# Optimization experiments

Measured on AMD Instinct MI355X. Metric: run time of the kernel, lower is better.

The kernel has to match this reference:

```python
import jax, jax.numpy as jnp
from jax import lax
import numpy as np

BETA = 0.5
ITERATION = 50
K = 1
EPS = 1e-5  # F.normalize eps


def cost_matrix_cosine(x, y):
    # x: [b,m,d], y: [b,n,d] -> cosine distance [b,m,n]
    xn = x / jnp.maximum(jnp.linalg.norm(x, axis=-1, keepdims=True), EPS)
    yn = y / jnp.maximum(jnp.linalg.norm(y, axis=-1, keepdims=True), EPS)
    return 1.0 - jnp.einsum('bmd,bnd->bmn', xn, yn)


def ipot(C, x_len, x_pad, y_len, y_pad, joint_pad, beta, iteration, k):
    # C: [b,m,n]; x_*: txt (m); y_*: img (n). Returns transport plan [b,m,n].
    b, m, n = C.shape
    jp_t = jnp.transpose(joint_pad, (0, 2, 1))                      # [b,n,m]
    A = jnp.where(jp_t, 0.0, jnp.exp(-jnp.transpose(C, (0, 2, 1)) / beta))
    T0 = jnp.where(jp_t, 0.0, 1.0)                                  # [b,n,m]
    sigma0 = jnp.where(x_pad, 0.0, 1.0 / x_len[:, None])[:, :, None]  # [b,m,1]
    x_mask = (x_pad.astype(C.dtype) * 1e4)[:, None, :]              # [b,1,m]
    y_mask = (y_pad.astype(C.dtype) * 1e4)[:, None, :]              # [b,1,n]
    xl = x_len[:, None, None]
    yl = y_len[:, None, None]

    def outer(carry, _):
        T, sigma = carry
        Q = A * T                                                   # [b,n,m]
        def inner(sig, _):
            # sig: [b,m,1]
            delta = 1.0 / (yl * jnp.transpose(jnp.matmul(Q, sig), (0, 2, 1)) + y_mask)  # [b,1,n]
            sig = jnp.transpose(1.0 / (xl * jnp.matmul(delta, Q) + x_mask), (0, 2, 1))  # [b,m,1]
            return sig, delta
        sigma, deltas = lax.scan(inner, sigma, None, length=k)
        delta = deltas[-1]                                          # [b,1,n]
        T = jnp.transpose(delta, (0, 2, 1)) * Q * jnp.transpose(sigma, (0, 2, 1))  # [b,n,m]
        return (T, sigma), None

    (T, _), _ = lax.scan(outer, (T0, sigma0), None, length=iteration)
    return jnp.transpose(T, (0, 2, 1))                              # [b,m,n]


def optimal_transport_dist(txt_emb, img_emb, txt_pad, img_pad):
    cost = cost_matrix_cosine(txt_emb, img_emb)                     # [b,m,n]
    joint_pad = txt_pad[:, :, None] | img_pad[:, None, :]           # [b,m,n]
    cost = jnp.where(joint_pad, 0.0, cost)
    txt_len = (txt_pad.shape[1] - jnp.sum(txt_pad, axis=1)).astype(cost.dtype)
    img_len = (img_pad.shape[1] - jnp.sum(img_pad, axis=1)).astype(cost.dtype)
    T = ipot(lax.stop_gradient(cost), txt_len, txt_pad, img_len, img_pad,
             joint_pad, BETA, ITERATION, K)
    # trace(cost @ T^T) == sum_ij cost_ij * plan_ij, per sample
    return jnp.sum(cost * lax.stop_gradient(T), axis=(1, 2))        # [b]


def reference(entitytxt_vec, object_vec, entitytxt_num, object_num):
    txt_nodes_emb = entitytxt_vec.astype(jnp.float32)               # [b,tl,d]
    img_nodes_emb = object_vec[:, 1:].astype(jnp.float32)           # [b,il,d]
    txt_pad = entitytxt_num == 0                                    # [b,tl] bool
    img_pad = object_num[:, 1:] == 0                                # [b,il] bool
    ot_dist = optimal_transport_dist(txt_nodes_emb, img_nodes_emb, txt_pad, img_pad)
    ot_loss = jnp.sum(ot_dist) * 0.01
    return ot_loss


def setup_inputs():
    key = jax.random.key(0)
    k1, k2, k3, k4 = jax.random.split(key, 4)
    b, tl, il1, d = 256, 128, 128, 1024
    entitytxt_vec = jax.random.normal(k1, (b, tl, d), dtype=jnp.float32)
    object_vec = jax.random.normal(k2, (b, il1, d), dtype=jnp.float32)
    entitytxt_num = jax.random.randint(k3, (b, tl), 0, 2, dtype=jnp.int32)
    object_num = jax.random.randint(k4, (b, il1), 0, 2, dtype=jnp.int32)
    # guarantee at least one valid node per sample (avoid 1/0 lengths)
    entitytxt_num = entitytxt_num.at[:, 0].set(1)
    object_num = object_num.at[:, 1].set(1)
    return {"entitytxt_vec": entitytxt_vec, "object_vec": object_vec,
            "entitytxt_num": entitytxt_num, "object_num": object_num}
```

## Files before the change

### kernel.cpp

```cpp
#include <hip/hip_runtime.h>
#include <math.h>

#define BATCH 256
#define M 128
#define NIMG 127
#define NP 128
#define D 1024
#define BK 64
#define NT (D / BK)
#define ITERS 50
#define LROW 72

typedef __attribute__((ext_vector_type(8))) short bf16x8;
typedef __attribute__((ext_vector_type(4))) float floatx4;

static __device__ __forceinline__ unsigned pack_bf16x2(float a, float b) {
    unsigned ua = __builtin_bit_cast(unsigned, a);
    unsigned ub = __builtin_bit_cast(unsigned, b);
    ua += 0x7fffu + ((ua >> 16) & 1u);
    ub += 0x7fffu + ((ub >> 16) & 1u);
    return (ua >> 16) | (ub & 0xffff0000u);
}

template<int CTRL>
static __device__ __forceinline__ float dpp_add(float v) {
    int s = __builtin_amdgcn_update_dpp(0, __builtin_bit_cast(int, v), CTRL, 0xf, 0xf, true);
    return v + __builtin_bit_cast(float, s);
}
static __device__ __forceinline__ float red16(float v) {
    v = dpp_add<0x121>(v);
    v = dpp_add<0x122>(v);
    v = dpp_add<0x124>(v);
    v = dpp_add<0x128>(v);
    return v;
}

static __device__ __forceinline__ void load_tile(const float* __restrict__ xb,
                                                 const float* __restrict__ yb,
                                                 int kk, int r0, int c16,
                                                 float4 (&vx)[4], float4 (&vy)[4]) {
#pragma unroll
    for (int it = 0; it < 4; ++it) {
        const int r = r0 + it * 32;
        vx[it] = *(const float4*)(xb + (size_t)r * D + kk + c16 * 4);
        float4 z = make_float4(0.f, 0.f, 0.f, 0.f);
        if (r < NIMG) z = *(const float4*)(yb + (size_t)r * D + kk + c16 * 4);
        vy[it] = z;
    }
}

static __device__ __forceinline__ void stage_tile(short* __restrict__ Xs, short* __restrict__ Ys,
                                                  int r0, int c16,
                                                  const float4 (&vx)[4], const float4 (&vy)[4],
                                                  float (&ssx)[4], float (&ssy)[4]) {
#pragma unroll
    for (int it = 0; it < 4; ++it) {
        const int r = r0 + it * 32;
        float4 v = vx[it];
        ssx[it] = fmaf(v.x, v.x, fmaf(v.y, v.y, fmaf(v.z, v.z, fmaf(v.w, v.w, ssx[it]))));
        uint2 p;
        p.x = pack_bf16x2(v.x, v.y);
        p.y = pack_bf16x2(v.z, v.w);
        *(uint2*)(&Xs[r * LROW + c16 * 4]) = p;
        v = vy[it];
        ssy[it] = fmaf(v.x, v.x, fmaf(v.y, v.y, fmaf(v.z, v.z, fmaf(v.w, v.w, ssy[it]))));
        p.x = pack_bf16x2(v.x, v.y);
        p.y = pack_bf16x2(v.z, v.w);
        *(uint2*)(&Ys[r * LROW + c16 * 4]) = p;
    }
}

static __device__ __forceinline__ void mfma_tile(const short* __restrict__ Xs,
                                                 const short* __restrict__ Ys,
                                                 int mbase, int nbase, int col, int quad,
                                                 floatx4 (&acc)[2][4]) {
#pragma unroll
    for (int ks = 0; ks < 2; ++ks) {
        const int koff = ks * 32 + quad * 8;
        bf16x8 af[2], bfr[4];
#pragma unroll
        for (int tr = 0; tr < 2; ++tr)
            af[tr] = *(const bf16x8*)(&Xs[(mbase + tr * 16 + col) * LROW + koff]);
#pragma unroll
        for (int tc = 0; tc < 4; ++tc)
            bfr[tc] = *(const bf16x8*)(&Ys[(nbase + tc * 16 + col) * LROW + koff]);
#pragma unroll
        for (int tr = 0; tr < 2; ++tr)
#pragma unroll
            for (int tc = 0; tc < 4; ++tc)
                acc[tr][tc] = __builtin_amdgcn_mfma_f32_16x16x32_bf16(
                    af[tr], bfr[tc], acc[tr][tc], 0, 0, 0);
    }
}

__launch_bounds__(512, 1)
__global__ void gemm_a_kernel(const float* __restrict__ xg,
                              const float* __restrict__ yg,
                              const int* __restrict__ xnum,
                              const int* __restrict__ ynum,
                              float* __restrict__ Aout)
{
    __shared__ __align__(16) short Xs[M * LROW];
    __shared__ __align__(16) short Ys[M * LROW];
    __shared__ __align__(16) float sinvx[M];
    __shared__ __align__(16) float sinvy[NP];
    __shared__ __align__(16) float sxmask[M];
    __shared__ __align__(16) float symask[NP];

    const int b    = blockIdx.x;
    const int t    = threadIdx.x;
    const int lane = t & 63;
    const int w    = t >> 6;

    const float* xb = xg + (size_t)b * M * D;
    const float* yb = yg + ((size_t)b * 128 + 1) * D;

    if (t < M)  sxmask[t] = (xnum[b * M + t] == 0) ? 1.0f : 0.0f;
    if (t < NP) symask[t] = (t < NIMG && ynum[b * 128 + t + 1] != 0) ? 0.0f : 1.0f;

    const int r0  = t >> 4;
    const int c16 = t & 15;

    floatx4 acc[2][4];
#pragma unroll
    for (int a = 0; a < 2; ++a)
#pragma unroll
        for (int c = 0; c < 4; ++c) acc[a][c] = (floatx4)0.0f;

    float ssx[4] = {0.f, 0.f, 0.f, 0.f};
    float ssy[4] = {0.f, 0.f, 0.f, 0.f};

    const int mbase = (w & 3) * 32;
    const int nbase = (w >> 2) * 64;
    const int col   = lane & 15;
    const int quad  = lane >> 4;

    float4 vxa[4], vya[4], vxb[4], vyb[4];
    load_tile(xb, yb, 0, r0, c16, vxa, vya);

#pragma unroll 1
    for (int ii = 0; ii < NT; ii += 2) {
        stage_tile(Xs, Ys, r0, c16, vxa, vya, ssx, ssy);
        load_tile(xb, yb, (ii + 1) * BK, r0, c16, vxb, vyb);
        __syncthreads();
        mfma_tile(Xs, Ys, mbase, nbase, col, quad, acc);
        __syncthreads();
        stage_tile(Xs, Ys, r0, c16, vxb, vyb, ssx, ssy);
        if (ii + 2 < NT) load_tile(xb, yb, (ii + 2) * BK, r0, c16, vxa, vya);
        __syncthreads();
        mfma_tile(Xs, Ys, mbase, nbase, col, quad, acc);
        __syncthreads();
    }

#pragma unroll
    for (int it = 0; it < 4; ++it) {
        ssx[it] = red16(ssx[it]);
        ssy[it] = red16(ssy[it]);
    }
    if (c16 == 0) {
#pragma unroll
        for (int it = 0; it < 4; ++it) {
            const int r = r0 + it * 32;
            sinvx[r] = 1.0f / fmaxf(sqrtf(ssx[it]), 1e-5f);
            sinvy[r] = 1.0f / fmaxf(sqrtf(ssy[it]), 1e-5f);
        }
    }
    __syncthreads();

    float* Ab = Aout + (size_t)b * M * NP;
#pragma unroll
    for (int tr = 0; tr < 2; ++tr)
#pragma unroll
        for (int tc = 0; tc < 4; ++tc) {
            const int n = nbase + tc * 16 + col;
            const float ivy_n = sinvy[n];
            const float ymf   = symask[n];
#pragma unroll
            for (int reg = 0; reg < 4; ++reg) {
                const int m = mbase + tr * 16 + quad * 4 + reg;
                const float p = acc[tr][tc][reg] * sinvx[m] * ivy_n;
                const float a = (sxmask[m] + ymf > 0.0f) ? 0.0f : expf(2.0f * p - 2.0f);
                Ab[m * NP + n] = a;
            }
        }
}

__launch_bounds__(512, 1)
__global__ void ipot_kernel(const float* __restrict__ Ain,
                            const int* __restrict__ xnum,
                            const int* __restrict__ ynum,
                            float* __restrict__ out)
{
    __shared__ __align__(16) float partCS[8 * 128];
    __shared__ __align__(16) float sdelta[NP];
    __shared__ __align__(16) float ssigma[M];
    __shared__ __align__(16) float sxmask[M];
    __shared__ __align__(16) float symask[NP];
    __shared__ float sxl_s, syl_s;
    __shared__ unsigned scnt[16];
    __shared__ float swsum[8];

    const int b    = blockIdx.x;
    const int t    = threadIdx.x;
    const int lane = t & 63;
    const int w    = t >> 6;
    const int tj   = t & 15;
    const int i0   = (t >> 4) * 4;
    const int j0   = tj * 8;

    bool tpad = true, ipad = true;
    if (t < M)  { tpad = (xnum[b * M + t] == 0); sxmask[t] = tpad ? 1e4f : 0.0f; }
    if (t < NP) { ipad = !(t < NIMG && ynum[b * 128 + t + 1] != 0); symask[t] = ipad ? 1e4f : 0.0f; }
    unsigned long long bx = __ballot(t < M  && !tpad);
    unsigned long long by = __ballot(t < NP && !ipad);
    if (lane == 0) { scnt[w] = (unsigned)__popcll(bx); scnt[8 + w] = (unsigned)__popcll(by); }
    __syncthreads();
    if (t == 0) {
        float xl = 0.f, yl = 0.f;
        for (int k = 0; k < 8; ++k) { xl += scnt[k]; yl += scnt[8 + k]; }
        sxl_s = xl; syl_s = yl;
    }
    __syncthreads();
    const float xl = sxl_s, yl = syl_s;
    if (t < M) ssigma[t] = tpad ? 0.0f : __builtin_amdgcn_rcpf(xl);

    const float* Ab = Ain + (size_t)b * M * NP;
    float Af[4][8], Q[4][8];
#pragma unroll
    for (int r = 0; r < 4; ++r) {
        float4 a0 = *(const float4*)(Ab + (size_t)(i0 + r) * NP + j0);
        float4 a1 = *(const float4*)(Ab + (size_t)(i0 + r) * NP + j0 + 4);
        Af[r][0] = a0.x; Af[r][1] = a0.y; Af[r][2] = a0.z; Af[r][3] = a0.w;
        Af[r][4] = a1.x; Af[r][5] = a1.y; Af[r][6] = a1.z; Af[r][7] = a1.w;
#pragma unroll
        for (int j = 0; j < 8; ++j) Q[r][j] = Af[r][j];
    }
    __syncthreads();

    float lp = 0.0f;
    for (int itn = 0; itn < ITERS; ++itn) {
        float sg[4];
        *(float4*)sg = *(const float4*)(&ssigma[i0]);
        float cp[8] = {0.f,0.f,0.f,0.f,0.f,0.f,0.f,0.f};
#pragma unroll
        for (int r = 0; r < 4; ++r)
#pragma unroll
            for (int j = 0; j < 8; ++j)
                cp[j] = fmaf(sg[r], Q[r][j], cp[j]);
#pragma unroll
        for (int j = 0; j < 8; ++j) {
            cp[j] += __shfl_xor(cp[j], 16);
            cp[j] += __shfl_xor(cp[j], 32);
        }
        if (lane < 16) {
            float4 c0 = make_float4(cp[0], cp[1], cp[2], cp[3]);
            float4 c1 = make_float4(cp[4], cp[5], cp[6], cp[7]);
            *(float4*)(&partCS[w * 128 + tj * 8])     = c0;
            *(float4*)(&partCS[w * 128 + tj * 8 + 4]) = c1;
        }
        __syncthreads();
        if (t < NP) {
            float s = 0.f;
#pragma unroll
            for (int w8 = 0; w8 < 8; ++w8) s += partCS[w8 * 128 + t];
            sdelta[t] = __builtin_amdgcn_rcpf(yl * s + symask[t]);
        }
        __syncthreads();
        float dl[8];
        *(float4*)dl       = *(const float4*)(&sdelta[j0]);
        *(float4*)(dl + 4) = *(const float4*)(&sdelta[j0 + 4]);
        float rp[4] = {0.f, 0.f, 0.f, 0.f};
#pragma unroll
        for (int r = 0; r < 4; ++r)
#pragma unroll
            for (int j = 0; j < 8; ++j)
                rp[r] = fmaf(dl[j], Q[r][j], rp[r]);
#pragma unroll
        for (int r = 0; r < 4; ++r) rp[r] = red16(rp[r]);
        if ((lane & 15) == 0) {
            float4 sv;
            sv.x = __builtin_amdgcn_rcpf(xl * rp[0] + sxmask[i0 + 0]);
            sv.y = __builtin_amdgcn_rcpf(xl * rp[1] + sxmask[i0 + 1]);
            sv.z = __builtin_amdgcn_rcpf(xl * rp[2] + sxmask[i0 + 2]);
            sv.w = __builtin_amdgcn_rcpf(xl * rp[3] + sxmask[i0 + 3]);
            *(float4*)(&ssigma[i0]) = sv;
        }
        __syncthreads();
        float sn[4];
        *(float4*)sn = *(const float4*)(&ssigma[i0]);
        if (itn < ITERS - 1) {
#pragma unroll
            for (int r = 0; r < 4; ++r) {
                const float f = sn[r];
#pragma unroll
                for (int j = 0; j < 8; ++j)
                    Q[r][j] *= Af[r][j] * dl[j] * f;
            }
        } else {
#pragma unroll
            for (int r = 0; r < 4; ++r)
#pragma unroll
                for (int j = 0; j < 8; ++j) {
                    const float a = Af[r][j];
                    if (a > 0.0f)
                        lp = fmaf(-0.5f * logf(a) * dl[j] * sn[r], Q[r][j], lp);
                }
        }
    }

#pragma unroll
    for (int off = 32; off > 0; off >>= 1) lp += __shfl_down(lp, off);
    if (lane == 0) swsum[w] = lp;
    __syncthreads();
    if (t == 0) {
        float tot = 0.f;
        for (int k = 0; k < 8; ++k) tot += swsum[k];
        atomicAdd(out, 0.01f * tot);
    }
}

extern "C" void kernel_launch(void* const* d_in, const int* in_sizes, int n_in,
                              void* d_out, int out_size, void* d_ws, size_t ws_size,
                              hipStream_t stream) {
    const float* x  = (const float*)d_in[0];
    const float* y  = (const float*)d_in[1];
    const int*   xn = (const int*)d_in[2];
    const int*   yn = (const int*)d_in[3];
    float* out = (float*)d_out;
    float* A   = (float*)d_ws;

    (void)hipMemsetAsync(out, 0, (size_t)out_size * sizeof(float), stream);
    gemm_a_kernel<<<dim3(BATCH), dim3(512), 0, stream>>>(x, y, xn, yn, A);
    ipot_kernel<<<dim3(BATCH), dim3(512), 0, stream>>>(A, xn, yn, out);
}
```

Before: 375.7 us.

## Split GEMM over image halves, double-buffer LDS, keep sigma in registers

```diff
diff --git a/kernel.cpp b/kernel.cpp
--- a/kernel.cpp
+++ b/kernel.cpp
@@ -10,6 +10,7 @@
 #define NT (D / BK)
 #define ITERS 50
 #define LROW 72
+#define NH 64
 
 typedef __attribute__((ext_vector_type(8))) short bf16x8;
 typedef __attribute__((ext_vector_type(4))) float floatx4;
@@ -37,22 +38,26 @@
 
 static __device__ __forceinline__ void load_tile(const float* __restrict__ xb,
                                                  const float* __restrict__ yb,
-                                                 int kk, int r0, int c16,
-                                                 float4 (&vx)[4], float4 (&vy)[4]) {
+                                                 int nh0, int kk, int r0, int c16,
+                                                 float4 (&vx)[4], float4 (&vy)[2]) {
 #pragma unroll
     for (int it = 0; it < 4; ++it) {
         const int r = r0 + it * 32;
         vx[it] = *(const float4*)(xb + (size_t)r * D + kk + c16 * 4);
+    }
+#pragma unroll
+    for (int it = 0; it < 2; ++it) {
+        const int r = r0 + it * 32;
         float4 z = make_float4(0.f, 0.f, 0.f, 0.f);
-        if (r < NIMG) z = *(const float4*)(yb + (size_t)r * D + kk + c16 * 4);
+        if (nh0 + r < NIMG) z = *(const float4*)(yb + (size_t)(nh0 + r) * D + kk + c16 * 4);
         vy[it] = z;
     }
 }
 
 static __device__ __forceinline__ void stage_tile(short* __restrict__ Xs, short* __restrict__ Ys,
                                                   int r0, int c16,
-                                                  const float4 (&vx)[4], const float4 (&vy)[4],
-                                                  float (&ssx)[4], float (&ssy)[4]) {
+                                                  const float4 (&vx)[4], const float4 (&vy)[2],
+                                                  float (&ssx)[4], float (&ssy)[2]) {
 #pragma unroll
     for (int it = 0; it < 4; ++it) {
         const int r = r0 + it * 32;
@@ -62,8 +67,13 @@
         p.x = pack_bf16x2(v.x, v.y);
         p.y = pack_bf16x2(v.z, v.w);
         *(uint2*)(&Xs[r * LROW + c16 * 4]) = p;
-        v = vy[it];
+    }
+#pragma unroll
+    for (int it = 0; it < 2; ++it) {
+        const int r = r0 + it * 32;
+        float4 v = vy[it];
         ssy[it] = fmaf(v.x, v.x, fmaf(v.y, v.y, fmaf(v.z, v.z, fmaf(v.w, v.w, ssy[it]))));
+        uint2 p;
         p.x = pack_bf16x2(v.x, v.y);
         p.y = pack_bf16x2(v.z, v.w);
         *(uint2*)(&Ys[r * LROW + c16 * 4]) = p;
@@ -73,41 +83,43 @@
 static __device__ __forceinline__ void mfma_tile(const short* __restrict__ Xs,
                                                  const short* __restrict__ Ys,
                                                  int mbase, int nbase, int col, int quad,
-                                                 floatx4 (&acc)[2][4]) {
+                                                 floatx4 (&acc)[2][2]) {
 #pragma unroll
     for (int ks = 0; ks < 2; ++ks) {
         const int koff = ks * 32 + quad * 8;
-        bf16x8 af[2], bfr[4];
+        bf16x8 af[2], bfr[2];
 #pragma unroll
         for (int tr = 0; tr < 2; ++tr)
             af[tr] = *(const bf16x8*)(&Xs[(mbase + tr * 16 + col) * LROW + koff]);
 #pragma unroll
-        for (int tc = 0; tc < 4; ++tc)
+        for (int tc = 0; tc < 2; ++tc)
             bfr[tc] = *(const bf16x8*)(&Ys[(nbase + tc * 16 + col) * LROW + koff]);
 #pragma unroll
         for (int tr = 0; tr < 2; ++tr)
 #pragma unroll
-            for (int tc = 0; tc < 4; ++tc)
+            for (int tc = 0; tc < 2; ++tc)
                 acc[tr][tc] = __builtin_amdgcn_mfma_f32_16x16x32_bf16(
                     af[tr], bfr[tc], acc[tr][tc], 0, 0, 0);
     }
 }
 
-__launch_bounds__(512, 1)
+__launch_bounds__(512, 4)
 __global__ void gemm_a_kernel(const float* __restrict__ xg,
                               const float* __restrict__ yg,
                               const int* __restrict__ xnum,
                               const int* __restrict__ ynum,
                               float* __restrict__ Aout)
 {
-    __shared__ __align__(16) short Xs[M * LROW];
-    __shared__ __align__(16) short Ys[M * LROW];
+    __shared__ __align__(16) short Xs[2][M * LROW];
+    __shared__ __align__(16) short Ys[2][NH * LROW];
     __shared__ __align__(16) float sinvx[M];
-    __shared__ __align__(16) float sinvy[NP];
+    __shared__ __align__(16) float sinvy[NH];
     __shared__ __align__(16) float sxmask[M];
-    __shared__ __align__(16) float symask[NP];
-
-    const int b    = blockIdx.x;
+    __shared__ __align__(16) float symask[NH];
+
+    const int bid  = blockIdx.x;
+    const int b    = bid & (BATCH - 1);
+    const int nh0  = (bid >> 8) * NH;
     const int t    = threadIdx.x;
     const int lane = t & 63;
     const int w    = t >> 6;
@@ -116,71 +128,72 @@
     const float* yb = yg + ((size_t)b * 128 + 1) * D;
 
     if (t < M)  sxmask[t] = (xnum[b * M + t] == 0) ? 1.0f : 0.0f;
-    if (t < NP) symask[t] = (t < NIMG && ynum[b * 128 + t + 1] != 0) ? 0.0f : 1.0f;
+    if (t < NH) {
+        const int n = nh0 + t;
+        symask[t] = (n < NIMG && ynum[b * 128 + n + 1] != 0) ? 0.0f : 1.0f;
+    }
 
     const int r0  = t >> 4;
     const int c16 = t & 15;
 
-    floatx4 acc[2][4];
+    floatx4 acc[2][2];
 #pragma unroll
     for (int a = 0; a < 2; ++a)
 #pragma unroll
-        for (int c = 0; c < 4; ++c) acc[a][c] = (floatx4)0.0f;
+        for (int c = 0; c < 2; ++c) acc[a][c] = (floatx4)0.0f;
 
     float ssx[4] = {0.f, 0.f, 0.f, 0.f};
-    float ssy[4] = {0.f, 0.f, 0.f, 0.f};
+    float ssy[2] = {0.f, 0.f};
 
     const int mbase = (w & 3) * 32;
-    const int nbase = (w >> 2) * 64;
+    const int nbase = (w >> 2) * 32;
     const int col   = lane & 15;
     const int quad  = lane >> 4;
 
-    float4 vxa[4], vya[4], vxb[4], vyb[4];
-    load_tile(xb, yb, 0, r0, c16, vxa, vya);
+    float4 vxa[4], vxb[4];
+    float4 vya[2], vyb[2];
+    load_tile(xb, yb, nh0, 0,  r0, c16, vxa, vya);
+    load_tile(xb, yb, nh0, BK, r0, c16, vxb, vyb);
 
 #pragma unroll 1
     for (int ii = 0; ii < NT; ii += 2) {
-        stage_tile(Xs, Ys, r0, c16, vxa, vya, ssx, ssy);
-        load_tile(xb, yb, (ii + 1) * BK, r0, c16, vxb, vyb);
+        stage_tile(Xs[0], Ys[0], r0, c16, vxa, vya, ssx, ssy);
+        if (ii + 2 < NT) load_tile(xb, yb, nh0, (ii + 2) * BK, r0, c16, vxa, vya);
         __syncthreads();
-        mfma_tile(Xs, Ys, mbase, nbase, col, quad, acc);
+        mfma_tile(Xs[0], Ys[0], mbase, nbase, col, quad, acc);
+        stage_tile(Xs[1], Ys[1], r0, c16, vxb, vyb, ssx, ssy);
+        if (ii + 3 < NT) load_tile(xb, yb, nh0, (ii + 3) * BK, r0, c16, vxb, vyb);
         __syncthreads();
-        stage_tile(Xs, Ys, r0, c16, vxb, vyb, ssx, ssy);
-        if (ii + 2 < NT) load_tile(xb, yb, (ii + 2) * BK, r0, c16, vxa, vya);
-        __syncthreads();
-        mfma_tile(Xs, Ys, mbase, nbase, col, quad, acc);
-        __syncthreads();
-    }
-
-#pragma unroll
-    for (int it = 0; it < 4; ++it) {
-        ssx[it] = red16(ssx[it]);
-        ssy[it] = red16(ssy[it]);
-    }
+        mfma_tile(Xs[1], Ys[1], mbase, nbase, col, quad, acc);
+    }
+
+#pragma unroll
+    for (int it = 0; it < 4; ++it) ssx[it] = red16(ssx[it]);
+#pragma unroll
+    for (int it = 0; it < 2; ++it) ssy[it] = red16(ssy[it]);
     if (c16 == 0) {
 #pragma unroll
-        for (int it = 0; it < 4; ++it) {
-            const int r = r0 + it * 32;
-            sinvx[r] = 1.0f / fmaxf(sqrtf(ssx[it]), 1e-5f);
-            sinvy[r] = 1.0f / fmaxf(sqrtf(ssy[it]), 1e-5f);
-        }
+        for (int it = 0; it < 4; ++it)
+            sinvx[r0 + it * 32] = 1.0f / fmaxf(sqrtf(ssx[it]), 1e-5f);
+#pragma unroll
+        for (int it = 0; it < 2; ++it)
+            sinvy[r0 + it * 32] = 1.0f / fmaxf(sqrtf(ssy[it]), 1e-5f);
     }
     __syncthreads();
 
-    float* Ab = Aout + (size_t)b * M * NP;
+    float* Ab = Aout + (size_t)b * M * NP + nh0;
 #pragma unroll
     for (int tr = 0; tr < 2; ++tr)
 #pragma unroll
-        for (int tc = 0; tc < 4; ++tc) {
-            const int n = nbase + tc * 16 + col;
-            const float ivy_n = sinvy[n];
-            const float ymf   = symask[n];
+        for (int tc = 0; tc < 2; ++tc) {
+            const int nl = nbase + tc * 16 + col;
+            const float ivy = sinvy[nl];
+            const float ymf = symask[nl];
 #pragma unroll
             for (int reg = 0; reg < 4; ++reg) {
                 const int m = mbase + tr * 16 + quad * 4 + reg;
-                const float p = acc[tr][tc][reg] * sinvx[m] * ivy_n;
-                const float a = (sxmask[m] + ymf > 0.0f) ? 0.0f : expf(2.0f * p - 2.0f);
-                Ab[m * NP + n] = a;
+                const float p = acc[tr][tc][reg] * sinvx[m] * ivy;
+                Ab[m * NP + nl] = (sxmask[m] + ymf > 0.0f) ? 0.0f : expf(2.0f * p - 2.0f);
             }
         }
 }
@@ -193,7 +206,6 @@
 {
     __shared__ __align__(16) float partCS[8 * 128];
     __shared__ __align__(16) float sdelta[NP];
-    __shared__ __align__(16) float ssigma[M];
     __shared__ __align__(16) float sxmask[M];
     __shared__ __align__(16) float symask[NP];
     __shared__ float sxl_s, syl_s;
@@ -222,7 +234,16 @@
     }
     __syncthreads();
     const float xl = sxl_s, yl = syl_s;
-    if (t < M) ssigma[t] = tpad ? 0.0f : __builtin_amdgcn_rcpf(xl);
+
+    float xm[4], ym[8];
+    *(float4*)xm       = *(const float4*)(&sxmask[i0]);
+    *(float4*)ym       = *(const float4*)(&symask[j0]);
+    *(float4*)(ym + 4) = *(const float4*)(&symask[j0 + 4]);
+
+    float sn[4];
+#pragma unroll
+    for (int r = 0; r < 4; ++r)
+        sn[r] = (xm[r] > 0.0f) ? 0.0f : __builtin_amdgcn_rcpf(xl);
 
     const float* Ab = Ain + (size_t)b * M * NP;
     float Af[4][8], Q[4][8];
@@ -235,18 +256,15 @@
 #pragma unroll
         for (int j = 0; j < 8; ++j) Q[r][j] = Af[r][j];
     }
-    __syncthreads();
 
     float lp = 0.0f;
     for (int itn = 0; itn < ITERS; ++itn) {
-        float sg[4];
-        *(float4*)sg = *(const float4*)(&ssigma[i0]);
         float cp[8] = {0.f,0.f,0.f,0.f,0.f,0.f,0.f,0.f};
 #pragma unroll
         for (int r = 0; r < 4; ++r)
 #pragma unroll
             for (int j = 0; j < 8; ++j)
-                cp[j] = fmaf(sg[r], Q[r][j], cp[j]);
+                cp[j] = fmaf(sn[r], Q[r][j], cp[j]);
 #pragma unroll
         for (int j = 0; j < 8; ++j) {
             cp[j] += __shfl_xor(cp[j], 16);
@@ -255,8 +273,8 @@
         if (lane < 16) {
             float4 c0 = make_float4(cp[0], cp[1], cp[2], cp[3]);
             float4 c1 = make_float4(cp[4], cp[5], cp[6], cp[7]);
-            *(float4*)(&partCS[w * 128 + tj * 8])     = c0;
-            *(float4*)(&partCS[w * 128 + tj * 8 + 4]) = c1;
+            *(float4*)(&partCS[w * 128 + j0])     = c0;
+            *(float4*)(&partCS[w * 128 + j0 + 4]) = c1;
         }
         __syncthreads();
         if (t < NP) {
@@ -277,17 +295,12 @@
                 rp[r] = fmaf(dl[j], Q[r][j], rp[r]);
 #pragma unroll
         for (int r = 0; r < 4; ++r) rp[r] = red16(rp[r]);
-        if ((lane & 15) == 0) {
-            float4 sv;
-            sv.x = __builtin_amdgcn_rcpf(xl * rp[0] + sxmask[i0 + 0]);
-            sv.y = __builtin_amdgcn_rcpf(xl * rp[1] + sxmask[i0 + 1]);
-            sv.z = __builtin_amdgcn_rcpf(xl * rp[2] + sxmask[i0 + 2]);
-            sv.w = __builtin_amdgcn_rcpf(xl * rp[3] + sxmask[i0 + 3]);
-            *(float4*)(&ssigma[i0]) = sv;
-        }
-        __syncthreads();
-        float sn[4];
-        *(float4*)sn = *(const float4*)(&ssigma[i0]);
+#pragma unroll
+        for (int r = 0; r < 4; ++r) rp[r] = __shfl(rp[r], lane & 48);
+#pragma unroll
+        for (int r = 0; r < 4; ++r)
+            sn[r] = __builtin_amdgcn_rcpf(xl * rp[r] + xm[r]);
+
         if (itn < ITERS - 1) {
 #pragma unroll
             for (int r = 0; r < 4; ++r) {
@@ -330,6 +343,6 @@
     float* A   = (float*)d_ws;
 
     (void)hipMemsetAsync(out, 0, (size_t)out_size * sizeof(float), stream);
-    gemm_a_kernel<<<dim3(BATCH), dim3(512), 0, stream>>>(x, y, xn, yn, A);
+    gemm_a_kernel<<<dim3(2 * BATCH), dim3(512), 0, stream>>>(x, y, xn, yn, A);
     ipot_kernel<<<dim3(BATCH), dim3(512), 0, stream>>>(A, xn, yn, out);
 }
```

Result: no change. 369.9 us (-1.6%).

## Double-buffer GEMM LDS tiles and keep IPOT sigma in registers

Applied to the files above, without the earlier changes.

```diff
diff --git a/kernel.cpp b/kernel.cpp
--- a/kernel.cpp
+++ b/kernel.cpp
@@ -33,6 +33,12 @@
     v = dpp_add<0x124>(v);
     v = dpp_add<0x128>(v);
     return v;
+}
+
+static __device__ __forceinline__ void barrier_lgkm() {
+    asm volatile("s_waitcnt lgkmcnt(0)" ::: "memory");
+    __builtin_amdgcn_s_barrier();
+    __builtin_amdgcn_sched_barrier(0);
 }
 
 static __device__ __forceinline__ void load_tile(const float* __restrict__ xb,
@@ -100,8 +106,8 @@
                               const int* __restrict__ ynum,
                               float* __restrict__ Aout)
 {
-    __shared__ __align__(16) short Xs[M * LROW];
-    __shared__ __align__(16) short Ys[M * LROW];
+    __shared__ __align__(16) short Xs[2][M * LROW];
+    __shared__ __align__(16) short Ys[2][M * LROW];
     __shared__ __align__(16) float sinvx[M];
     __shared__ __align__(16) float sinvy[NP];
     __shared__ __align__(16) float sxmask[M];
@@ -136,20 +142,19 @@
     const int quad  = lane >> 4;
 
     float4 vxa[4], vya[4], vxb[4], vyb[4];
-    load_tile(xb, yb, 0, r0, c16, vxa, vya);
+    load_tile(xb, yb, 0,  r0, c16, vxa, vya);
+    load_tile(xb, yb, BK, r0, c16, vxb, vyb);
 
 #pragma unroll 1
     for (int ii = 0; ii < NT; ii += 2) {
-        stage_tile(Xs, Ys, r0, c16, vxa, vya, ssx, ssy);
-        load_tile(xb, yb, (ii + 1) * BK, r0, c16, vxb, vyb);
-        __syncthreads();
-        mfma_tile(Xs, Ys, mbase, nbase, col, quad, acc);
-        __syncthreads();
-        stage_tile(Xs, Ys, r0, c16, vxb, vyb, ssx, ssy);
+        stage_tile(Xs[0], Ys[0], r0, c16, vxa, vya, ssx, ssy);
         if (ii + 2 < NT) load_tile(xb, yb, (ii + 2) * BK, r0, c16, vxa, vya);
-        __syncthreads();
-        mfma_tile(Xs, Ys, mbase, nbase, col, quad, acc);
-        __syncthreads();
+        barrier_lgkm();
+        mfma_tile(Xs[0], Ys[0], mbase, nbase, col, quad, acc);
+        stage_tile(Xs[1], Ys[1], r0, c16, vxb, vyb, ssx, ssy);
+        if (ii + 3 < NT) load_tile(xb, yb, (ii + 3) * BK, r0, c16, vxb, vyb);
+        barrier_lgkm();
+        mfma_tile(Xs[1], Ys[1], mbase, nbase, col, quad, acc);
     }
 
 #pragma unroll
@@ -165,7 +170,7 @@
             sinvy[r] = 1.0f / fmaxf(sqrtf(ssy[it]), 1e-5f);
         }
     }
-    __syncthreads();
+    barrier_lgkm();
 
     float* Ab = Aout + (size_t)b * M * NP;
 #pragma unroll
@@ -193,7 +198,6 @@
 {
     __shared__ __align__(16) float partCS[8 * 128];
     __shared__ __align__(16) float sdelta[NP];
-    __shared__ __align__(16) float ssigma[M];
     __shared__ __align__(16) float sxmask[M];
     __shared__ __align__(16) float symask[NP];
     __shared__ float sxl_s, syl_s;
@@ -222,7 +226,16 @@
     }
     __syncthreads();
     const float xl = sxl_s, yl = syl_s;
-    if (t < M) ssigma[t] = tpad ? 0.0f : __builtin_amdgcn_rcpf(xl);
+
+    float xm[4], ym[8];
+    *(float4*)xm       = *(const float4*)(&sxmask[i0]);
+    *(float4*)ym       = *(const float4*)(&symask[j0]);
+    *(float4*)(ym + 4) = *(const float4*)(&symask[j0 + 4]);
+
+    float sn[4];
+#pragma unroll
+    for (int r = 0; r < 4; ++r)
+        sn[r] = (xm[r] > 0.0f) ? 0.0f : __builtin_amdgcn_rcpf(xl);
 
     const float* Ab = Ain + (size_t)b * M * NP;
     float Af[4][8], Q[4][8];
@@ -235,18 +248,15 @@
 #pragma unroll
         for (int j = 0; j < 8; ++j) Q[r][j] = Af[r][j];
     }
-    __syncthreads();
 
     float lp = 0.0f;
     for (int itn = 0; itn < ITERS; ++itn) {
-        float sg[4];
-        *(float4*)sg = *(const float4*)(&ssigma[i0]);
         float cp[8] = {0.f,0.f,0.f,0.f,0.f,0.f,0.f,0.f};
 #pragma unroll
         for (int r = 0; r < 4; ++r)
 #pragma unroll
             for (int j = 0; j < 8; ++j)
-                cp[j] = fmaf(sg[r], Q[r][j], cp[j]);
+                cp[j] = fmaf(sn[r], Q[r][j], cp[j]);
 #pragma unroll
         for (int j = 0; j < 8; ++j) {
             cp[j] += __shfl_xor(cp[j], 16);
@@ -255,8 +265,8 @@
         if (lane < 16) {
             float4 c0 = make_float4(cp[0], cp[1], cp[2], cp[3]);
             float4 c1 = make_float4(cp[4], cp[5], cp[6], cp[7]);
-            *(float4*)(&partCS[w * 128 + tj * 8])     = c0;
-            *(float4*)(&partCS[w * 128 + tj * 8 + 4]) = c1;
+            *(float4*)(&partCS[w * 128 + j0])     = c0;
+            *(float4*)(&partCS[w * 128 + j0 + 4]) = c1;
         }
         __syncthreads();
         if (t < NP) {
@@ -277,17 +287,12 @@
                 rp[r] = fmaf(dl[j], Q[r][j], rp[r]);
 #pragma unroll
         for (int r = 0; r < 4; ++r) rp[r] = red16(rp[r]);
-        if ((lane & 15) == 0) {
-            float4 sv;
-            sv.x = __builtin_amdgcn_rcpf(xl * rp[0] + sxmask[i0 + 0]);
-            sv.y = __builtin_amdgcn_rcpf(xl * rp[1] + sxmask[i0 + 1]);
-            sv.z = __builtin_amdgcn_rcpf(xl * rp[2] + sxmask[i0 + 2]);
-            sv.w = __builtin_amdgcn_rcpf(xl * rp[3] + sxmask[i0 + 3]);
-            *(float4*)(&ssigma[i0]) = sv;
-        }
-        __syncthreads();
-        float sn[4];
-        *(float4*)sn = *(const float4*)(&ssigma[i0]);
+#pragma unroll
+        for (int r = 0; r < 4; ++r) rp[r] = __shfl(rp[r], lane & 48);
+#pragma unroll
+        for (int r = 0; r < 4; ++r)
+            sn[r] = __builtin_amdgcn_rcpf(xl * rp[r] + xm[r]);
+
         if (itn < ITERS - 1) {
 #pragma unroll
             for (int r = 0; r < 4; ++r) {
```

New measurement: 346.8 us. 1.08x faster.
